# Kernel optimization log

Hardware: AMD Instinct MI355X
Metric: run time of the kernel (lower is better)

Reference implementation:

```python
import jax, jax.numpy as jnp
import numpy as np

N, D, V = 4096, 512, 100000


def setup_inputs() -> dict:
    key = jax.random.key(0)
    k1, k2, k3 = jax.random.split(key, 3)
    x = jax.random.normal(k1, (N, D), dtype=jnp.float32)
    lb = jax.random.randint(k2, (N,), 0, V, dtype=jnp.int64)
    W = jax.random.normal(k3, (V, D), dtype=jnp.float32) * 0.02
    b = jnp.zeros((V,), dtype=jnp.float32)
    return {"x": x, "lb": lb, "W": W, "b": b}


def reference(x, lb, W, b):
    # fc: logits[N, V] = x @ W^T + b
    logits = jnp.einsum('nd,vd->nv', x, W) + b
    # numerically-stable softmax cross-entropy, mean reduction
    logz = jax.nn.logsumexp(logits, axis=-1)               # [N]
    tgt = jnp.take_along_axis(logits, lb[:, None], axis=-1)[:, 0]  # [N]
    loss = jnp.mean(logz - tgt)
    return loss
```

## Files before the change

kernel.cpp:

```cpp
#include <hip/hip_runtime.h>
#include <hip/hip_bf16.h>
#include <math.h>


#define N_ROWS 4096
#define DIM    512
#define VOCAB  100000
#define NTILES 782
#define VPAD   (NTILES * 128)
#define SPLITS 32
#define TPS    25
#define XELEMS (N_ROWS * DIM)
#define WVALID ((size_t)VOCAB * DIM)
#define WBYTES ((size_t)VPAD * DIM)
#define TILEB  (128 * DIM)
#define PREP_BLOCKS 4096
#define PREP_F4     ((XELEMS + WBYTES) / 4)

#define LOG2E 1.44269504088896340736f

typedef __attribute__((ext_vector_type(4))) int   i32x4;
typedef __attribute__((ext_vector_type(8))) int   i32x8;
typedef __attribute__((ext_vector_type(4))) float f32x4;


__device__ __forceinline__ void gload_lds16(const char* g, char* l) {
  __builtin_amdgcn_global_load_lds(
      (const __attribute__((address_space(1))) unsigned int*)g,
      (__attribute__((address_space(3))) unsigned int*)l, 16, 0, 0);
}

__device__ __forceinline__ int pack4_fp8(float4 f, float sc) {
  int p = __builtin_amdgcn_cvt_pk_fp8_f32(f.x * sc, f.y * sc, 0, false);
  p = __builtin_amdgcn_cvt_pk_fp8_f32(f.z * sc, f.w * sc, p, true);
  return p;
}

__device__ __forceinline__ i32x8 frag32(const char* base) {
  i32x4 lo = *(const i32x4*)(base);
  i32x4 hi = *(const i32x4*)(base + 1024);
  return (i32x8){lo.x, lo.y, lo.z, lo.w, hi.x, hi.y, hi.z, hi.w};
}


__global__ __launch_bounds__(256) void prep_kernel(const float* __restrict__ x,
                                                   const float* __restrict__ W,
                                                   char* __restrict__ out8,
                                                   const int* __restrict__ lb,
                                                   const float* __restrict__ bias,
                                                   float* __restrict__ tgt) {
  if (blockIdx.x < PREP_BLOCKS) {
    for (size_t i4 = (size_t)blockIdx.x * 256 + threadIdx.x; i4 < (size_t)PREP_F4;
         i4 += (size_t)PREP_BLOCKS * 256) {
      const size_t f0 = i4 * 4;
      if (f0 < (size_t)XELEMS) {
        *(int*)(out8 + f0) = pack4_fp8(*(const float4*)(x + f0), LOG2E);
      } else {
        const size_t wf = f0 - XELEMS;
        int o = 0;
        if (wf < WVALID) o = pack4_fp8(*(const float4*)(W + wf), 32.f);
        const unsigned v  = (unsigned)(wf >> 9);
        const unsigned dd = (unsigned)(wf & 511);
        const unsigned out = ((v >> 7) << 16)
                           + ((dd >> 7) << 14)
                           + (((v >> 4) & 7u) << 11)
                           + (((dd >> 4) & 1u) << 10)
                           + (((dd >> 5) & 3u) << 8)
                           + ((v & 15u) << 4)
                           + (dd & 15u);
        *(int*)(out8 + XELEMS + out) = o;
      }
    }
  } else {
    const int wv = threadIdx.x >> 6;
    const int lane = threadIdx.x & 63;
    const int row = (blockIdx.x - PREP_BLOCKS) * 4 + wv;
    const int t = lb[row];
    const float* xr = x + (size_t)row * DIM;
    const float* wr = W + (size_t)t * DIM;
    float s = 0.f;
#pragma unroll
    for (int i = 0; i < 8; ++i) s += xr[lane + i * 64] * wr[lane + i * 64];
#pragma unroll
    for (int m = 32; m; m >>= 1) s += __shfl_xor(s, m);
    if (lane == 0) tgt[row] = s + bias[t];
  }
}


__global__ __launch_bounds__(256, 2) void lse_kernel(const char* __restrict__ xb,
                                                     const char* __restrict__ wb,
                                                     const float* __restrict__ bias,
                                                     float* __restrict__ spart) {
  __shared__ __align__(16) char ldsB[4][2][8192];
  __shared__ float ldsBias[TPS * 128];

  const int d = blockIdx.x;
  const int s     = 2 * (d & 7) + ((d >> 3) & 1) + 16 * (d >> 9);
  const int mtile = (d >> 4) & 31;

  const int m0 = mtile * 128;
  const int t0 = s * TPS;
  const int t1 = (t0 + TPS < NTILES) ? (t0 + TPS) : NTILES;
  const int NT = t1 - t0;

  const int tid  = threadIdx.x;
  const int lane = tid & 63;
  const int wv   = tid >> 6;
  const int rh   = wv >> 1;
  const int ch   = wv & 1;
  const int fr   = lane & 15;
  const int fq   = lane >> 4;

  i32x8 Aa[4][4];
  {
    const char* ax = xb + (size_t)(m0 + 64 * rh + fr) * DIM + fq * 32;
#pragma unroll
    for (int rf = 0; rf < 4; ++rf)
#pragma unroll
      for (int ks = 0; ks < 4; ++ks) {
        const char* p = ax + rf * (16 * DIM) + ks * 128;
        i32x4 lo = *(const i32x4*)p;
        i32x4 hi = *(const i32x4*)(p + 16);
        Aa[rf][ks] = (i32x8){lo.x, lo.y, lo.z, lo.w, hi.x, hi.y, hi.z, hi.w};
      }
  }

  for (int c = tid; c < NT * 128; c += 256) {
    const int col = t0 * 128 + c;
    ldsBias[c] = (col < VOCAB) ? bias[col] * LOG2E : -INFINITY;
  }
  __syncthreads();
  asm volatile("s_waitcnt vmcnt(0)" ::: "memory");
  __builtin_amdgcn_sched_barrier(0);

  char* const myB  = &ldsB[wv][0][0];
  char* const buf0 = myB;
  char* const buf1 = myB + 8192;

  auto stageK = [&](const char* tileSrc, int ks, char* dst) {
    const char* src = tileSrc + ks * 16384 + ch * 8192 + lane * 16;
#pragma unroll
    for (int j = 0; j < 8; ++j)
      gload_lds16(src + j * 1024, dst + j * 1024);
  };

  float S[4][4];
#pragma unroll
  for (int rf = 0; rf < 4; ++rf)
#pragma unroll
    for (int r = 0; r < 4; ++r) S[rf][r] = 0.f;

  f32x4 acc[4][4];

#define K_STEP(ksC, FIRSTF, WAITIMM, STAGE_EXPR)                              \
  {                                                                           \
    asm volatile("s_waitcnt vmcnt(" #WAITIMM ")" ::: "memory");               \
    __builtin_amdgcn_sched_barrier(0);                                        \
    const char* fb_ = myB + ((ksC) & 1) * 8192 + lane * 16;                   \
    __builtin_amdgcn_s_setprio(1);                                            \
    _Pragma("unroll")                                                         \
    for (int gg_ = 0; gg_ < 4; ++gg_) {                                       \
      const i32x8 bf_ = frag32(fb_ + gg_ * 2048);                             \
      _Pragma("unroll")                                                       \
      for (int rf_ = 0; rf_ < 4; ++rf_)                                       \
        acc[rf_][gg_] = __builtin_amdgcn_mfma_scale_f32_16x16x128_f8f6f4(     \
            Aa[rf_][ksC], bf_,                                                \
            (FIRSTF) ? (f32x4){0.f, 0.f, 0.f, 0.f} : acc[rf_][gg_],           \
            0, 0, 0, 127, 0, 122);                                            \
    }                                                                         \
    __builtin_amdgcn_s_setprio(0);                                            \
    asm volatile("s_waitcnt lgkmcnt(0)" ::: "memory");                        \
    __builtin_amdgcn_sched_barrier(0);                                        \
    STAGE_EXPR;                                                               \
  }

  auto epilogue = [&](int ti) {
    const float* bT = &ldsBias[ti * 128 + 64 * ch];
    float badd[4];
#pragma unroll
    for (int c = 0; c < 4; ++c) badd[c] = bT[16 * c + fr];
#pragma unroll
    for (int rf = 0; rf < 4; ++rf)
#pragma unroll
      for (int r = 0; r < 4; ++r) {
        float sum = 0.f;
#pragma unroll
        for (int c = 0; c < 4; ++c)
          sum += __builtin_amdgcn_exp2f(acc[rf][c][r] + badd[c]);
        S[rf][r] += sum;
      }
  };

  const char* wt = wb + (size_t)t0 * TILEB;

  stageK(wt, 0, buf0);
  stageK(wt, 1, buf1);

  for (int tt = t0; tt < t1 - 1; ++tt, wt += TILEB) {
    K_STEP(0, true,  8, stageK(wt, 2, buf0))
    K_STEP(1, false, 8, stageK(wt, 3, buf1))
    K_STEP(2, false, 8, stageK(wt + TILEB, 0, buf0))
    K_STEP(3, false, 8, stageK(wt + TILEB, 1, buf1))
    epilogue(tt - t0);
  }

  {
    K_STEP(0, true,  8, stageK(wt, 2, buf0))
    K_STEP(1, false, 8, stageK(wt, 3, buf1))
    K_STEP(2, false, 8, (void)0)
    K_STEP(3, false, 0, (void)0)
    epilogue(NT - 1);
  }
#undef K_STEP

  __syncthreads();
  float* sc = (float*)ldsB;
  if (ch == 1) {
    float* base = sc + (size_t)(rh * 64 + lane) * 20;
#pragma unroll
    for (int rf = 0; rf < 4; ++rf)
      *(float4*)(base + rf * 4) = (float4){S[rf][0], S[rf][1], S[rf][2], S[rf][3]};
  }
  __syncthreads();
  if (ch == 0) {
    const float* base = sc + (size_t)(rh * 64 + lane) * 20;
#pragma unroll
    for (int rf = 0; rf < 4; ++rf) {
      const float4 v = *(const float4*)(base + rf * 4);
      S[rf][0] += v.x; S[rf][1] += v.y; S[rf][2] += v.z; S[rf][3] += v.w;
    }
#pragma unroll
    for (int rf = 0; rf < 4; ++rf)
#pragma unroll
      for (int r = 0; r < 4; ++r) {
        float v = S[rf][r];
        v += __shfl_xor(v, 1);
        v += __shfl_xor(v, 2);
        v += __shfl_xor(v, 4);
        v += __shfl_xor(v, 8);
        if (fr == 0) {
          const int row = m0 + 64 * rh + 16 * rf + 4 * fq + r;
          spart[(size_t)row * SPLITS + s] = v;
        }
      }
  }
}


__global__ __launch_bounds__(256) void combine_kernel(const float* __restrict__ spart,
                                                      const float* __restrict__ tgt,
                                                      float* __restrict__ out) {
  __shared__ float red[256];
  float local = 0.f;
  for (int r = threadIdx.x; r < N_ROWS; r += 256) {
    const float4* sp = (const float4*)(spart + (size_t)r * SPLITS);
    float st = 0.f;
#pragma unroll
    for (int i = 0; i < 8; ++i) { float4 v = sp[i]; st += (v.x + v.y) + (v.z + v.w); }
    local += __logf(st) - tgt[r];
  }
  red[threadIdx.x] = local;
  __syncthreads();
  for (int step = 128; step; step >>= 1) {
    if (threadIdx.x < step) red[threadIdx.x] += red[threadIdx.x + step];
    __syncthreads();
  }
  if (threadIdx.x == 0) out[0] = red[0] * (1.0f / (float)N_ROWS);
}


extern "C" void kernel_launch(void* const* d_in, const int* in_sizes, int n_in,
                              void* d_out, int out_size, void* d_ws, size_t ws_size,
                              hipStream_t stream) {
  const float* x  = (const float*)d_in[0];
  const int*   lb = (const int*)d_in[1];
  const float* W  = (const float*)d_in[2];
  const float* b  = (const float*)d_in[3];
  float* out = (float*)d_out;

  char* ws = (char*)d_ws;
  const size_t OFF_W   = (size_t)XELEMS;
  const size_t OFF_SP  = OFF_W + WBYTES;
  const size_t OFF_TGT = OFF_SP + (size_t)N_ROWS * SPLITS * 4;
  char*  xb    = ws;
  char*  wb    = ws + OFF_W;
  float* spart = (float*)(ws + OFF_SP);
  float* tgt   = (float*)(ws + OFF_TGT);

  prep_kernel<<<PREP_BLOCKS + 1024, 256, 0, stream>>>(x, W, ws, lb, b, tgt);
  lse_kernel<<<1024, 256, 0, stream>>>(xb, wb, b, spart);
  combine_kernel<<<1, 256, 0, stream>>>(spart, tgt, out);
}
```

Baseline: 536.2 us.

## Split LSE blocks by column half, share B tiles across waves via barrier

Each lse_kernel block now handles one 64-column half for a row tile using 2 waves, with 2048 blocks of 128 threads and a new XCD-aware block-to-work mapping. The two waves cooperatively stage a 4-buffer shared LDS ring with a workgroup barrier per K step, replacing per-wave private double buffers. Bias is loaded per tile into a register and broadcast with shuffles instead of being preloaded into LDS, and the cross-wave LDS reduction is removed by writing 64 partials per row, which the combine kernel now sums. This raises occupancy and trims LDS use, at the cost of extra barriers and twice as many partial sums.

Measured after the change: 597.8 us. +11.5%, slower.

```diff
diff --git a/kernel.cpp b/kernel.cpp
--- a/kernel.cpp
+++ b/kernel.cpp
@@ -9,6 +9,7 @@
 #define NTILES 782
 #define VPAD   (NTILES * 128)
 #define SPLITS 32
+#define NPART  64
 #define TPS    25
 #define XELEMS (N_ROWS * DIM)
 #define WVALID ((size_t)VOCAB * DIM)
@@ -22,6 +23,9 @@
 typedef __attribute__((ext_vector_type(4))) int   i32x4;
 typedef __attribute__((ext_vector_type(8))) int   i32x8;
 typedef __attribute__((ext_vector_type(4))) float f32x4;
+
+#define WAITN(n) asm volatile("s_waitcnt vmcnt(" #n ")" ::: "memory")
+#define SB0()    __builtin_amdgcn_sched_barrier(0)
 
 
 __device__ __forceinline__ void gload_lds16(const char* g, char* l) {
@@ -88,27 +92,27 @@
 }
 
 
-__global__ __launch_bounds__(256, 2) void lse_kernel(const char* __restrict__ xb,
+__global__ __launch_bounds__(128, 2) void lse_kernel(const char* __restrict__ xb,
                                                      const char* __restrict__ wb,
                                                      const float* __restrict__ bias,
                                                      float* __restrict__ spart) {
-  __shared__ __align__(16) char ldsB[4][2][8192];
-  __shared__ float ldsBias[TPS * 128];
-
-  const int d = blockIdx.x;
-  const int s     = 2 * (d & 7) + ((d >> 3) & 1) + 16 * (d >> 9);
-  const int mtile = (d >> 4) & 31;
+  __shared__ __align__(16) char ldsB[4][8192];
+
+  const int i    = blockIdx.x;
+  const int xcd  = i & 7;
+  const int slot = i >> 3;
+  const int g    = 8 * xcd + (slot >> 5);
+  const int mtile = slot & 31;
+  const int s  = g >> 1;
+  const int ch = g & 1;
 
   const int m0 = mtile * 128;
   const int t0 = s * TPS;
   const int t1 = (t0 + TPS < NTILES) ? (t0 + TPS) : NTILES;
-  const int NT = t1 - t0;
 
   const int tid  = threadIdx.x;
   const int lane = tid & 63;
-  const int wv   = tid >> 6;
-  const int rh   = wv >> 1;
-  const int ch   = wv & 1;
+  const int rh   = tid >> 6;
   const int fr   = lane & 15;
   const int fq   = lane >> 4;
 
@@ -125,23 +129,13 @@
         Aa[rf][ks] = (i32x8){lo.x, lo.y, lo.z, lo.w, hi.x, hi.y, hi.z, hi.w};
       }
   }
-
-  for (int c = tid; c < NT * 128; c += 256) {
-    const int col = t0 * 128 + c;
-    ldsBias[c] = (col < VOCAB) ? bias[col] * LOG2E : -INFINITY;
-  }
-  __syncthreads();
-  asm volatile("s_waitcnt vmcnt(0)" ::: "memory");
-  __builtin_amdgcn_sched_barrier(0);
-
-  char* const myB  = &ldsB[wv][0][0];
-  char* const buf0 = myB;
-  char* const buf1 = myB + 8192;
-
-  auto stageK = [&](const char* tileSrc, int ks, char* dst) {
-    const char* src = tileSrc + ks * 16384 + ch * 8192 + lane * 16;
-#pragma unroll
-    for (int j = 0; j < 8; ++j)
+  WAITN(0); SB0();
+
+  auto stageK = [&](const char* tileSrc, int ks, char* buf) {
+    const char* src = tileSrc + ks * 16384 + ch * 8192 + rh * 4096 + lane * 16;
+    char* dst = buf + rh * 4096;
+#pragma unroll
+    for (int j = 0; j < 4; ++j)
       gload_lds16(src + j * 1024, dst + j * 1024);
   };
 
@@ -152,12 +146,16 @@
     for (int r = 0; r < 4; ++r) S[rf][r] = 0.f;
 
   f32x4 acc[4][4];
-
-#define K_STEP(ksC, FIRSTF, WAITIMM, STAGE_EXPR)                              \
+  float biasv = 0.f;
+
+#define K_STEP(ksC, FIRSTF, WAITIMM, STAGE_EXPR, BIAS_EXPR)                   \
   {                                                                           \
-    asm volatile("s_waitcnt vmcnt(" #WAITIMM ")" ::: "memory");               \
-    __builtin_amdgcn_sched_barrier(0);                                        \
-    const char* fb_ = myB + ((ksC) & 1) * 8192 + lane * 16;                   \
+    WAITN(WAITIMM); SB0();                                                    \
+    __builtin_amdgcn_s_barrier(); SB0();                                      \
+    STAGE_EXPR;                                                               \
+    SB0();            \
+    BIAS_EXPR;                                                                \
+    const char* fb_ = &ldsB[(ksC)][0] + lane * 16;                            \
     __builtin_amdgcn_s_setprio(1);                                            \
     _Pragma("unroll")                                                         \
     for (int gg_ = 0; gg_ < 4; ++gg_) {                                       \
@@ -170,16 +168,14 @@
             0, 0, 0, 127, 0, 122);                                            \
     }                                                                         \
     __builtin_amdgcn_s_setprio(0);                                            \
-    asm volatile("s_waitcnt lgkmcnt(0)" ::: "memory");                        \
-    __builtin_amdgcn_sched_barrier(0);                                        \
-    STAGE_EXPR;                                                               \
-  }
-
-  auto epilogue = [&](int ti) {
-    const float* bT = &ldsBias[ti * 128 + 64 * ch];
+  }
+
+  auto epilogue = [&](int tt) {
+    const int cbase = tt * 128 + 64 * ch;
+    const float bvt = (cbase + lane < VOCAB) ? biasv * LOG2E : -INFINITY;
     float badd[4];
 #pragma unroll
-    for (int c = 0; c < 4; ++c) badd[c] = bT[16 * c + fr];
+    for (int c = 0; c < 4; ++c) badd[c] = __shfl(bvt, 16 * c + fr, 64);
 #pragma unroll
     for (int rf = 0; rf < 4; ++rf)
 #pragma unroll
@@ -194,57 +190,45 @@
 
   const char* wt = wb + (size_t)t0 * TILEB;
 
-  stageK(wt, 0, buf0);
-  stageK(wt, 1, buf1);
+  stageK(wt, 0, ldsB[0]);
+  stageK(wt, 1, ldsB[1]);
 
   for (int tt = t0; tt < t1 - 1; ++tt, wt += TILEB) {
-    K_STEP(0, true,  8, stageK(wt, 2, buf0))
-    K_STEP(1, false, 8, stageK(wt, 3, buf1))
-    K_STEP(2, false, 8, stageK(wt + TILEB, 0, buf0))
-    K_STEP(3, false, 8, stageK(wt + TILEB, 1, buf1))
-    epilogue(tt - t0);
+    const int bcol = tt * 128 + 64 * ch + lane;
+    K_STEP(0, true,  4, stageK(wt, 2, ldsB[2]),
+           biasv = bias[bcol < VOCAB ? bcol : (VOCAB - 1)])
+    K_STEP(1, false, 5, stageK(wt, 3, ldsB[3]), (void)0)
+    K_STEP(2, false, 5, stageK(wt + TILEB, 0, ldsB[0]), (void)0)
+    K_STEP(3, false, 4, stageK(wt + TILEB, 1, ldsB[1]), (void)0)
+    epilogue(tt);
   }
 
   {
-    K_STEP(0, true,  8, stageK(wt, 2, buf0))
-    K_STEP(1, false, 8, stageK(wt, 3, buf1))
-    K_STEP(2, false, 8, (void)0)
-    K_STEP(3, false, 0, (void)0)
-    epilogue(NT - 1);
+    const int tt = t1 - 1;
+    const int bcol = tt * 128 + 64 * ch + lane;
+    K_STEP(0, true,  4, stageK(wt, 2, ldsB[2]),
+           biasv = bias[bcol < VOCAB ? bcol : (VOCAB - 1)])
+    K_STEP(1, false, 5, stageK(wt, 3, ldsB[3]), (void)0)
+    K_STEP(2, false, 5, (void)0, (void)0)
+    K_STEP(3, false, 0, (void)0, (void)0)
+    epilogue(tt);
   }
 #undef K_STEP
 
-  __syncthreads();
-  float* sc = (float*)ldsB;
-  if (ch == 1) {
-    float* base = sc + (size_t)(rh * 64 + lane) * 20;
-#pragma unroll
-    for (int rf = 0; rf < 4; ++rf)
-      *(float4*)(base + rf * 4) = (float4){S[rf][0], S[rf][1], S[rf][2], S[rf][3]};
-  }
-  __syncthreads();
-  if (ch == 0) {
-    const float* base = sc + (size_t)(rh * 64 + lane) * 20;
-#pragma unroll
-    for (int rf = 0; rf < 4; ++rf) {
-      const float4 v = *(const float4*)(base + rf * 4);
-      S[rf][0] += v.x; S[rf][1] += v.y; S[rf][2] += v.z; S[rf][3] += v.w;
+#pragma unroll
+  for (int rf = 0; rf < 4; ++rf)
+#pragma unroll
+    for (int r = 0; r < 4; ++r) {
+      float v = S[rf][r];
+      v += __shfl_xor(v, 1);
+      v += __shfl_xor(v, 2);
+      v += __shfl_xor(v, 4);
+      v += __shfl_xor(v, 8);
+      if (fr == 0) {
+        const int row = m0 + 64 * rh + 16 * rf + 4 * fq + r;
+        spart[(size_t)row * NPART + (s * 2 + ch)] = v;
+      }
     }
-#pragma unroll
-    for (int rf = 0; rf < 4; ++rf)
-#pragma unroll
-      for (int r = 0; r < 4; ++r) {
-        float v = S[rf][r];
-        v += __shfl_xor(v, 1);
-        v += __shfl_xor(v, 2);
-        v += __shfl_xor(v, 4);
-        v += __shfl_xor(v, 8);
-        if (fr == 0) {
-          const int row = m0 + 64 * rh + 16 * rf + 4 * fq + r;
-          spart[(size_t)row * SPLITS + s] = v;
-        }
-      }
-  }
 }
 
 
@@ -254,10 +238,10 @@
   __shared__ float red[256];
   float local = 0.f;
   for (int r = threadIdx.x; r < N_ROWS; r += 256) {
-    const float4* sp = (const float4*)(spart + (size_t)r * SPLITS);
+    const float4* sp = (const float4*)(spart + (size_t)r * NPART);
     float st = 0.f;
 #pragma unroll
-    for (int i = 0; i < 8; ++i) { float4 v = sp[i]; st += (v.x + v.y) + (v.z + v.w); }
+    for (int i = 0; i < 16; ++i) { float4 v = sp[i]; st += (v.x + v.y) + (v.z + v.w); }
     local += __logf(st) - tgt[r];
   }
   red[threadIdx.x] = local;
@@ -282,13 +266,13 @@
   char* ws = (char*)d_ws;
   const size_t OFF_W   = (size_t)XELEMS;
   const size_t OFF_SP  = OFF_W + WBYTES;
-  const size_t OFF_TGT = OFF_SP + (size_t)N_ROWS * SPLITS * 4;
+  const size_t OFF_TGT = OFF_SP + (size_t)N_ROWS * NPART * 4;
   char*  xb    = ws;
   char*  wb    = ws + OFF_W;
   float* spart = (float*)(ws + OFF_SP);
   float* tgt   = (float*)(ws + OFF_TGT);
 
   prep_kernel<<<PREP_BLOCKS + 1024, 256, 0, stream>>>(x, W, ws, lb, b, tgt);
-  lse_kernel<<<1024, 256, 0, stream>>>(xb, wb, b, spart);
+  lse_kernel<<<2048, 128, 0, stream>>>(xb, wb, b, spart);
   combine_kernel<<<1, 256, 0, stream>>>(spart, tgt, out);
 }
```
